# Optimization experiments

Hardware: AMD Instinct MI355X
Metric: run time of the kernel (lower is better)

Reference implementation:

```python
import jax, jax.numpy as jnp
import numpy as np

H, KV, D, HID = 36, 4, 128, 4608   # heads, kv heads, head_dim, hidden
THETA = 100000.0
NEG = -1e30


def _rope_neox(pos, x):
    # pos: [T] int, x: [T, nh, D]; neox style: rotate half
    half = D // 2
    inv_freq = 1.0 / (THETA ** (jnp.arange(half, dtype=jnp.float32) / half))
    ang = pos.astype(jnp.float32)[:, None] * inv_freq          # [T, half]
    cos = jnp.cos(ang)[:, None, :]
    sin = jnp.sin(ang)[:, None, :]
    x1, x2 = x[..., :half], x[..., half:]
    return jnp.concatenate([x1 * cos - x2 * sin, x2 * cos + x1 * sin], axis=-1)


def setup_inputs() -> dict:
    key = jax.random.key(0)
    ks = jax.random.split(key, 6)
    T = 2048
    return {
        "positions": jnp.arange(T, dtype=jnp.int32),
        "hidden_states": jax.random.normal(ks[0], (T, HID), dtype=jnp.float32),
        "wqkv": jax.random.normal(ks[1], (H * D + 2 * KV * D, HID), dtype=jnp.float32) * 0.02,
        "bqkv": jax.random.normal(ks[2], (H * D + 2 * KV * D,), dtype=jnp.float32) * 0.02,
        "wo": jax.random.normal(ks[3], (HID, H * D), dtype=jnp.float32) * 0.02,
        "bo": jax.random.normal(ks[4], (HID,), dtype=jnp.float32) * 0.02,
        "window": 1024,
    }


def reference(positions, hidden_states, wqkv, bqkv, wo, bo, window):
    T = hidden_states.shape[0]
    qkv = hidden_states @ wqkv.T + bqkv                         # [T, 5632]
    q, k, v = jnp.split(qkv, [H * D, H * D + KV * D], axis=-1)
    q = q.reshape(T, H, D)
    k = k.reshape(T, KV, D)
    v = v.reshape(T, KV, D)
    q = _rope_neox(positions, q)
    k = _rope_neox(positions, k)
    # GQA: expand kv heads to query heads
    g = H // KV
    k = jnp.repeat(k, g, axis=1)                                # [T, H, D]
    v = jnp.repeat(v, g, axis=1)
    scale = D ** -0.5
    scores = jnp.einsum('thd,shd->hts', q, k) * scale           # [H, T, T]
    t = jnp.arange(T)
    # causal + sliding window: attend to s in (t - window, t]
    mask = (t[None, :] <= t[:, None]) & (t[None, :] > t[:, None] - window)
    scores = jnp.where(mask[None, :, :], scores, NEG)
    p = jax.nn.softmax(scores, axis=-1)
    attn = jnp.einsum('hts,shd->thd', p, v).reshape(T, H * D)
    return attn @ wo.T + bo
```

## Files before the change

### kernel.cpp

```cpp
#include <hip/hip_runtime.h>
#include <hip/hip_bf16.h>
#include <math.h>


#define T_SEQ   2048
#define HIDDEN  4608
#define NHEAD   36
#define NKVH    4
#define HEADDIM 128
#define GQA_G   9
#define NQKV    5632
#define KOFF    4608
#define VOFF    5120
#define NEG_BIG -1e30f
#define BQ 64
#define BS 32
#define NTILE   64
#define PSTR 40

typedef short bf16x8 __attribute__((ext_vector_type(8)));
typedef float f32x4  __attribute__((ext_vector_type(4)));

__device__ inline bf16x8 pack8(float4 u, float4 v) {
    union { bf16x8 v8; __hip_bfloat162 h[4]; } r;
    r.h[0] = __float22bfloat162_rn(make_float2(u.x, u.y));
    r.h[1] = __float22bfloat162_rn(make_float2(u.z, u.w));
    r.h[2] = __float22bfloat162_rn(make_float2(v.x, v.y));
    r.h[3] = __float22bfloat162_rn(make_float2(v.z, v.w));
    return r.v8;
}

typedef const __attribute__((address_space(1))) int* gas_ptr;
typedef __attribute__((address_space(3))) int*       las_ptr;
__device__ __forceinline__ void gload_lds16(const void* g, void* l) {
    __builtin_amdgcn_global_load_lds((gas_ptr)g, (las_ptr)l, 16, 0, 0);
}

__global__ __launch_bounds__(256)
void cvt_bf16_kernel(const float* __restrict__ in, __hip_bfloat16* __restrict__ out,
                     int n8)
{
    for (int i = blockIdx.x * 256 + threadIdx.x; i < n8; i += gridDim.x * 256) {
        const float4 a = *(const float4*)(in + (size_t)i * 8);
        const float4 b = *(const float4*)(in + (size_t)i * 8 + 4);
        *(bf16x8*)(out + (size_t)i * 8) = pack8(a, b);
    }
}

__global__ __launch_bounds__(256)
void gemm_bf16bt_kernel(const __hip_bfloat16* __restrict__ A,
                        const __hip_bfloat16* __restrict__ B,
                        const float* __restrict__ bias,
                        float* __restrict__ C, int N, int K)
{
    __shared__ short As[128 * 32];
    __shared__ short Bs[128 * 32];

    const int tid  = threadIdx.x;
    const int lane = tid & 63;
    const int wave = tid >> 6;
    const int row0 = blockIdx.y * 128;
    const int col0 = blockIdx.x * 128;
    const int wr   = (wave >> 1) * 64;
    const int wc   = (wave & 1) * 64;
    const int fr   = lane & 15;
    const int fk   = (lane >> 4) * 8;

    const int srow = lane >> 2;
    const int scol = (lane & 3) * 8;

    const __hip_bfloat16* Ag0 = A + (size_t)(row0 + wave * 32 + srow) * K + scol;
    const __hip_bfloat16* Ag1 = Ag0 + (size_t)16 * K;
    const __hip_bfloat16* Bg0 = B + (size_t)(col0 + wave * 32 + srow) * K + scol;
    const __hip_bfloat16* Bg1 = Bg0 + (size_t)16 * K;

    short* Al0 = &As[(wave * 32) * 32];
    short* Al1 = &As[(wave * 32 + 16) * 32];
    short* Bl0 = &Bs[(wave * 32) * 32];
    short* Bl1 = &Bs[(wave * 32 + 16) * 32];

    f32x4 acc[4][4];
    #pragma unroll
    for (int i = 0; i < 4; ++i)
        #pragma unroll
        for (int j = 0; j < 4; ++j)
            #pragma unroll
            for (int r = 0; r < 4; ++r) acc[i][j][r] = 0.0f;

    for (int k0 = 0; k0 < K; k0 += 32) {
        __syncthreads();
        gload_lds16(Ag0 + k0, Al0);
        gload_lds16(Ag1 + k0, Al1);
        gload_lds16(Bg0 + k0, Bl0);
        gload_lds16(Bg1 + k0, Bl1);
        __syncthreads();

        bf16x8 af[4], bfr[4];
        #pragma unroll
        for (int i = 0; i < 4; ++i)
            af[i] = *(const bf16x8*)&As[(wr + i * 16 + fr) * 32 + fk];
        #pragma unroll
        for (int j = 0; j < 4; ++j)
            bfr[j] = *(const bf16x8*)&Bs[(wc + j * 16 + fr) * 32 + fk];

        #pragma unroll
        for (int i = 0; i < 4; ++i)
            #pragma unroll
            for (int j = 0; j < 4; ++j)
                acc[i][j] = __builtin_amdgcn_mfma_f32_16x16x32_bf16(
                    af[i], bfr[j], acc[i][j], 0, 0, 0);
    }

    const int quad = lane >> 4;
    #pragma unroll
    for (int j = 0; j < 4; ++j) {
        const int col = col0 + wc + j * 16 + fr;
        const float bv = bias[col];
        #pragma unroll
        for (int i = 0; i < 4; ++i) {
            const int rowb = row0 + wr + i * 16 + quad * 4;
            #pragma unroll
            for (int r = 0; r < 4; ++r)
                C[(size_t)(rowb + r) * N + col] = acc[i][j][r] + bv;
        }
    }
}

__global__ __launch_bounds__(256)
void prep_kv_kernel(const int* __restrict__ positions,
                    const float* __restrict__ qkv,
                    __hip_bfloat16* __restrict__ Kht,
                    __hip_bfloat16* __restrict__ Klt,
                    __hip_bfloat16* __restrict__ Vtt)
{
    const int tile = blockIdx.x;
    const int kvh  = blockIdx.y;
    const int t    = threadIdx.x;
    const size_t ib = ((size_t)kvh * NTILE + tile) * 4096;

    {
        const int s   = t >> 3;
        const int j8  = (t & 7) * 8;
        const int row = tile * BS + s;
        const float* kp = qkv + (size_t)row * NQKV + KOFF + kvh * HEADDIM;
        float x1[8], x2[8];
        *(float4*)&x1[0] = *(const float4*)(kp + j8);
        *(float4*)&x1[4] = *(const float4*)(kp + j8 + 4);
        *(float4*)&x2[0] = *(const float4*)(kp + 64 + j8);
        *(float4*)&x2[4] = *(const float4*)(kp + 64 + j8 + 4);
        const float pos = (float)positions[row];
        union { bf16x8 v; __hip_bfloat16 x[8]; } H1, L1, H2, L2;
        #pragma unroll
        for (int j = 0; j < 8; ++j) {
            const int d = j8 + j;
            const float inv_freq = __expf(-(float)d * (11.512925465f / 64.0f));
            float sn, cs;
            sincosf(pos * inv_freq, &sn, &cs);
            const float r1 = x1[j] * cs - x2[j] * sn;
            const float r2 = x2[j] * cs + x1[j] * sn;
            const __hip_bfloat16 h1 = __float2bfloat16(r1);
            const __hip_bfloat16 h2 = __float2bfloat16(r2);
            H1.x[j] = h1; L1.x[j] = __float2bfloat16(r1 - __bfloat162float(h1));
            H2.x[j] = h2; L2.x[j] = __float2bfloat16(r2 - __bfloat162float(h2));
        }
        const int gd1 = (t & 7);
        const int gd2 = gd1 + 8;
        *(bf16x8*)&Kht[ib + gd1 * 256 + s * 8] = H1.v;
        *(bf16x8*)&Kht[ib + gd2 * 256 + s * 8] = H2.v;
        *(bf16x8*)&Klt[ib + gd1 * 256 + s * 8] = L1.v;
        *(bf16x8*)&Klt[ib + gd2 * 256 + s * 8] = L2.v;
    }

    {
        const int q  = t >> 6;
        const int d0 = (t & 63) * 2;
        const float* vp = qkv + (size_t)(tile * BS + q * 8) * NQKV + VOFF
                        + kvh * HEADDIM + d0;
        union { bf16x8 v; __hip_bfloat16 x[8]; } V0, V1;
        #pragma unroll
        for (int j = 0; j < 8; ++j) {
            const float2 vv = *(const float2*)(vp + (size_t)j * NQKV);
            const __hip_bfloat162 pb = __float22bfloat162_rn(make_float2(vv.x, vv.y));
            V0.x[j] = pb.x;
            V1.x[j] = pb.y;
        }
        *(bf16x8*)&Vtt[ib + q * 1024 + d0 * 8]       = V0.v;
        *(bf16x8*)&Vtt[ib + q * 1024 + (d0 + 1) * 8] = V1.v;
    }
}

__global__ __launch_bounds__(256)
void attn_kernel(const float* __restrict__ qkv,
                 const int* __restrict__ positions,
                 const __hip_bfloat16* __restrict__ Kht,
                 const __hip_bfloat16* __restrict__ Klt,
                 const __hip_bfloat16* __restrict__ Vtt,
                 __hip_bfloat16* __restrict__ out,
                 const int* __restrict__ windowp)
{
    __shared__ short KhS[2][4096];
    __shared__ short KlS[2][4096];
    __shared__ short VtS[2][4096];
    __shared__ __hip_bfloat16 Ps[4][16 * PSTR];

    const int h    = blockIdx.x;
    const int q0   = blockIdx.y * BQ;
    const int kvh  = h / GQA_G;
    const int tid  = threadIdx.x;
    const int lane = tid & 63;
    const int wave = tid >> 6;
    const int l15  = lane & 15;
    const int quad = lane >> 4;
    const int window = *windowp;
    const float scale = 0.088388347648318447f;

    bf16x8 qh[4], ql[4];
    {
        const int qrow = q0 + wave * 16 + l15;
        const float* qp = qkv + (size_t)qrow * NQKV + h * HEADDIM + quad * 8;
        float qv[32];
        #pragma unroll
        for (int ks = 0; ks < 4; ++ks) {
            *(float4*)&qv[ks * 8]     = *(const float4*)(qp + ks * 32);
            *(float4*)&qv[ks * 8 + 4] = *(const float4*)(qp + ks * 32 + 4);
        }
        const float pos = (float)positions[qrow];
        #pragma unroll
        for (int p = 0; p < 2; ++p)
            #pragma unroll
            for (int j = 0; j < 8; ++j) {
                const int d = p * 32 + quad * 8 + j;
                const float inv_freq = __expf(-(float)d * (11.512925465f / 64.0f));
                float sn, cs;
                sincosf(pos * inv_freq, &sn, &cs);
                const float x1 = qv[p * 8 + j];
                const float x2 = qv[(p + 2) * 8 + j];
                qv[p * 8 + j]       = x1 * cs - x2 * sn;
                qv[(p + 2) * 8 + j] = x2 * cs + x1 * sn;
            }
        #pragma unroll
        for (int ks = 0; ks < 4; ++ks) {
            union { bf16x8 v; __hip_bfloat16 x[8]; } H, L;
            #pragma unroll
            for (int j = 0; j < 8; ++j) {
                const float v = qv[ks * 8 + j] * scale;
                const __hip_bfloat16 hb = __float2bfloat16(v);
                H.x[j] = hb;
                L.x[j] = __float2bfloat16(v - __bfloat162float(hb));
            }
            qh[ks] = H.v; ql[ks] = L.v;
        }
    }

    f32x4 o[8];
    #pragma unroll
    for (int c = 0; c < 8; ++c)
        #pragma unroll
        for (int r = 0; r < 4; ++r) o[c][r] = 0.0f;
    float mrun[4], lrun[4];
    #pragma unroll
    for (int r = 0; r < 4; ++r) { mrun[r] = NEG_BIG; lrun[r] = 0.0f; }

    int s_lo = q0 - window + 1;
    if (s_lo < 0) s_lo = 0;
    s_lo &= ~(BS - 1);
    const int tile0  = s_lo >> 5;
    const int ntiles = ((q0 + BQ) - s_lo) >> 5;

    const short* gKh = (const short*)Kht + ((size_t)kvh * NTILE) * 4096;
    const short* gKl = (const short*)Klt + ((size_t)kvh * NTILE) * 4096;
    const short* gVt = (const short*)Vtt + ((size_t)kvh * NTILE) * 4096;

    __hip_bfloat16* Psw = &Ps[wave][0];

    auto STAGE = [&](int buf, int tile) {
        const size_t toff = (size_t)tile * 4096;
        #pragma unroll
        for (int i = 0; i < 2; ++i) {
            const int o = (wave * 2 + i) * 512;
            gload_lds16(gKh + toff + o + lane * 8, &KhS[buf][o]);
            gload_lds16(gKl + toff + o + lane * 8, &KlS[buf][o]);
            gload_lds16(gVt + toff + o + lane * 8, &VtS[buf][o]);
        }
    };

    STAGE(0, tile0);
    __syncthreads();
    int cur = 0;

    for (int it = 0; it < ntiles; ++it) {
        const int st = s_lo + it * BS;
        if (it + 1 < ntiles) STAGE(cur ^ 1, tile0 + it + 1);

        f32x4 acc0, acc1;
        #pragma unroll
        for (int r = 0; r < 4; ++r) { acc0[r] = 0.0f; acc1[r] = 0.0f; }
        #pragma unroll
        for (int ks = 0; ks < 4; ++ks) {
            const int g = (ks * 4 + quad) * 256;
            const bf16x8 bh0 = *(const bf16x8*)&KhS[cur][g + l15 * 8];
            const bf16x8 bl0 = *(const bf16x8*)&KlS[cur][g + l15 * 8];
            const bf16x8 bh1 = *(const bf16x8*)&KhS[cur][g + (16 + l15) * 8];
            const bf16x8 bl1 = *(const bf16x8*)&KlS[cur][g + (16 + l15) * 8];
            acc0 = __builtin_amdgcn_mfma_f32_16x16x32_bf16(qh[ks], bh0, acc0, 0, 0, 0);
            acc1 = __builtin_amdgcn_mfma_f32_16x16x32_bf16(qh[ks], bh1, acc1, 0, 0, 0);
            acc0 = __builtin_amdgcn_mfma_f32_16x16x32_bf16(ql[ks], bh0, acc0, 0, 0, 0);
            acc1 = __builtin_amdgcn_mfma_f32_16x16x32_bf16(ql[ks], bh1, acc1, 0, 0, 0);
            acc0 = __builtin_amdgcn_mfma_f32_16x16x32_bf16(qh[ks], bl0, acc0, 0, 0, 0);
            acc1 = __builtin_amdgcn_mfma_f32_16x16x32_bf16(qh[ks], bl1, acc1, 0, 0, 0);
        }

        const int qb  = q0 + wave * 16 + quad * 4;
        const int s0g = st + l15;
        const int s1g = st + 16 + l15;
        #pragma unroll
        for (int r = 0; r < 4; ++r) {
            const int q = qb + r;
            const bool v0 = (s0g <= q) && (s0g > q - window);
            const bool v1 = (s1g <= q) && (s1g > q - window);
            float a = v0 ? acc0[r] : NEG_BIG;
            float b = v1 ? acc1[r] : NEG_BIG;
            float mx = fmaxf(a, b);
            mx = fmaxf(mx, __shfl_xor(mx, 1));
            mx = fmaxf(mx, __shfl_xor(mx, 2));
            mx = fmaxf(mx, __shfl_xor(mx, 4));
            mx = fmaxf(mx, __shfl_xor(mx, 8));
            mx = fmaxf(mrun[r], mx);
            const float alpha = __expf(mrun[r] - mx);
            mrun[r] = mx;
            const float e0 = v0 ? __expf(acc0[r] - mx) : 0.0f;
            const float e1 = v1 ? __expf(acc1[r] - mx) : 0.0f;
            const __hip_bfloat162 pp = __float22bfloat162_rn(make_float2(e0, e1));
            Psw[(quad * 4 + r) * PSTR + l15]      = pp.x;
            Psw[(quad * 4 + r) * PSTR + 16 + l15] = pp.y;
            float sum = __bfloat162float(pp.x) + __bfloat162float(pp.y);
            sum += __shfl_xor(sum, 1);
            sum += __shfl_xor(sum, 2);
            sum += __shfl_xor(sum, 4);
            sum += __shfl_xor(sum, 8);
            lrun[r] = lrun[r] * alpha + sum;
            #pragma unroll
            for (int c = 0; c < 8; ++c) o[c][r] *= alpha;
        }

        const bf16x8 pa = *(const bf16x8*)&Psw[l15 * PSTR + quad * 8];
        #pragma unroll
        for (int c = 0; c < 8; ++c) {
            const bf16x8 vb = *(const bf16x8*)&VtS[cur][quad * 1024 + (16 * c + l15) * 8];
            o[c] = __builtin_amdgcn_mfma_f32_16x16x32_bf16(pa, vb, o[c], 0, 0, 0);
        }

        __syncthreads();
        cur ^= 1;
    }

    #pragma unroll
    for (int r = 0; r < 4; ++r) {
        const float inv = 1.0f / lrun[r];
        __hip_bfloat16* op = out
                  + (size_t)(q0 + wave * 16 + quad * 4 + r) * (NHEAD * HEADDIM)
                  + h * HEADDIM + l15;
        #pragma unroll
        for (int c = 0; c < 8; ++c) op[16 * c] = __float2bfloat16(o[c][r] * inv);
    }
}

extern "C" void kernel_launch(void* const* d_in, const int* in_sizes, int n_in,
                              void* d_out, int out_size, void* d_ws, size_t ws_size,
                              hipStream_t stream)
{
    const int*   positions = (const int*)d_in[0];
    const float* hidden    = (const float*)d_in[1];
    const float* wqkv      = (const float*)d_in[2];
    const float* bqkv      = (const float*)d_in[3];
    const float* wo        = (const float*)d_in[4];
    const float* bo        = (const float*)d_in[5];
    const int*   windowp   = (const int*)d_in[6];
    float* outp = (float*)d_out;

    float* qkv = (float*)d_ws;
    __hip_bfloat16* hbf  = (__hip_bfloat16*)(qkv + (size_t)T_SEQ * NQKV);
    __hip_bfloat16* wqbf = hbf  + (size_t)T_SEQ * HIDDEN;
    __hip_bfloat16* wobf = wqbf + (size_t)NQKV * HIDDEN;
    __hip_bfloat16* abf  = wobf + (size_t)HIDDEN * HIDDEN;
    __hip_bfloat16* Kht  = abf  + (size_t)T_SEQ * HIDDEN;
    __hip_bfloat16* Klt  = Kht  + (size_t)NKVH * NTILE * 4096;
    __hip_bfloat16* Vtt  = Klt  + (size_t)NKVH * NTILE * 4096;

    cvt_bf16_kernel<<<1024, 256, 0, stream>>>(hidden, hbf, T_SEQ * HIDDEN / 8);
    cvt_bf16_kernel<<<2048, 256, 0, stream>>>(wqkv, wqbf, NQKV * HIDDEN / 8);
    cvt_bf16_kernel<<<2048, 256, 0, stream>>>(wo, wobf, HIDDEN * HIDDEN / 8);

    gemm_bf16bt_kernel<<<dim3(NQKV / 128, T_SEQ / 128), 256, 0, stream>>>(
        hbf, wqbf, bqkv, qkv, NQKV, HIDDEN);

    prep_kv_kernel<<<dim3(NTILE, NKVH), 256, 0, stream>>>(
        positions, qkv, Kht, Klt, Vtt);

    attn_kernel<<<dim3(NHEAD, T_SEQ / BQ), 256, 0, stream>>>(
        qkv, positions, Kht, Klt, Vtt, abf, windowp);

    gemm_bf16bt_kernel<<<dim3(HIDDEN / 128, T_SEQ / 128), 256, 0, stream>>>(
        abf, wobf, bo, outp, HIDDEN, HIDDEN);
}
```

Baseline: 717.8 us.

## Switch attention to fp16 single-pass MFMA, lazy rescale, and deepen GEMM K-step

Attention drops the bf16 hi/lo split of Q and K, which needed three MFMAs per product, and uses a single fp16 MFMA instead. It also folds log2(e) into the scale to use exp2, and skips the online-softmax rescale unless the row max grows by more than a threshold. The attention grid is reversed so the heaviest query blocks launch first, and the GEMM now loads 64 K-elements per barrier pair using two LDS buffers. The fp16 path trades accuracy for speed, with overflow risk if values exceed the fp16 range, and the lazy rescale lets exponentials reach up to 2^8 before renormalising.

```diff
diff --git a/kernel.cpp b/kernel.cpp
--- a/kernel.cpp
+++ b/kernel.cpp
@@ -18,8 +18,9 @@
 #define NTILE   64
 #define PSTR 40
 
-typedef short bf16x8 __attribute__((ext_vector_type(8)));
-typedef float f32x4  __attribute__((ext_vector_type(4)));
+typedef short    bf16x8 __attribute__((ext_vector_type(8)));
+typedef _Float16 f16x8  __attribute__((ext_vector_type(8)));
+typedef float    f32x4  __attribute__((ext_vector_type(4)));
 
 __device__ inline bf16x8 pack8(float4 u, float4 v) {
     union { bf16x8 v8; __hip_bfloat162 h[4]; } r;
@@ -53,8 +54,8 @@
                         const float* __restrict__ bias,
                         float* __restrict__ C, int N, int K)
 {
-    __shared__ short As[128 * 32];
-    __shared__ short Bs[128 * 32];
+    __shared__ short As[2][128 * 32];
+    __shared__ short Bs[2][128 * 32];
 
     const int tid  = threadIdx.x;
     const int lane = tid & 63;
@@ -69,15 +70,8 @@
     const int srow = lane >> 2;
     const int scol = (lane & 3) * 8;
 
-    const __hip_bfloat16* Ag0 = A + (size_t)(row0 + wave * 32 + srow) * K + scol;
-    const __hip_bfloat16* Ag1 = Ag0 + (size_t)16 * K;
-    const __hip_bfloat16* Bg0 = B + (size_t)(col0 + wave * 32 + srow) * K + scol;
-    const __hip_bfloat16* Bg1 = Bg0 + (size_t)16 * K;
-
-    short* Al0 = &As[(wave * 32) * 32];
-    short* Al1 = &As[(wave * 32 + 16) * 32];
-    short* Bl0 = &Bs[(wave * 32) * 32];
-    short* Bl1 = &Bs[(wave * 32 + 16) * 32];
+    const __hip_bfloat16* Ag = A + (size_t)(row0 + wave * 32 + srow) * K + scol;
+    const __hip_bfloat16* Bg = B + (size_t)(col0 + wave * 32 + srow) * K + scol;
 
     f32x4 acc[4][4];
     #pragma unroll
@@ -87,28 +81,36 @@
             #pragma unroll
             for (int r = 0; r < 4; ++r) acc[i][j][r] = 0.0f;
 
-    for (int k0 = 0; k0 < K; k0 += 32) {
+    for (int k0 = 0; k0 < K; k0 += 64) {
         __syncthreads();
-        gload_lds16(Ag0 + k0, Al0);
-        gload_lds16(Ag1 + k0, Al1);
-        gload_lds16(Bg0 + k0, Bl0);
-        gload_lds16(Bg1 + k0, Bl1);
+        #pragma unroll
+        for (int kk = 0; kk < 2; ++kk)
+            #pragma unroll
+            for (int i = 0; i < 2; ++i) {
+                gload_lds16(Ag + k0 + kk * 32 + (size_t)(i * 16) * K,
+                            &As[kk][(wave * 32 + i * 16) * 32]);
+                gload_lds16(Bg + k0 + kk * 32 + (size_t)(i * 16) * K,
+                            &Bs[kk][(wave * 32 + i * 16) * 32]);
+            }
         __syncthreads();
 
-        bf16x8 af[4], bfr[4];
-        #pragma unroll
-        for (int i = 0; i < 4; ++i)
-            af[i] = *(const bf16x8*)&As[(wr + i * 16 + fr) * 32 + fk];
-        #pragma unroll
-        for (int j = 0; j < 4; ++j)
-            bfr[j] = *(const bf16x8*)&Bs[(wc + j * 16 + fr) * 32 + fk];
-
-        #pragma unroll
-        for (int i = 0; i < 4; ++i)
+        #pragma unroll
+        for (int kk = 0; kk < 2; ++kk) {
+            bf16x8 af[4], bfr[4];
+            #pragma unroll
+            for (int i = 0; i < 4; ++i)
+                af[i] = *(const bf16x8*)&As[kk][(wr + i * 16 + fr) * 32 + fk];
             #pragma unroll
             for (int j = 0; j < 4; ++j)
-                acc[i][j] = __builtin_amdgcn_mfma_f32_16x16x32_bf16(
-                    af[i], bfr[j], acc[i][j], 0, 0, 0);
+                bfr[j] = *(const bf16x8*)&Bs[kk][(wc + j * 16 + fr) * 32 + fk];
+
+            #pragma unroll
+            for (int i = 0; i < 4; ++i)
+                #pragma unroll
+                for (int j = 0; j < 4; ++j)
+                    acc[i][j] = __builtin_amdgcn_mfma_f32_16x16x32_bf16(
+                        af[i], bfr[j], acc[i][j], 0, 0, 0);
+        }
     }
 
     const int quad = lane >> 4;
@@ -129,9 +131,8 @@
 __global__ __launch_bounds__(256)
 void prep_kv_kernel(const int* __restrict__ positions,
                     const float* __restrict__ qkv,
-                    __hip_bfloat16* __restrict__ Kht,
-                    __hip_bfloat16* __restrict__ Klt,
-                    __hip_bfloat16* __restrict__ Vtt)
+                    _Float16* __restrict__ Kt,
+                    _Float16* __restrict__ Vt)
 {
     const int tile = blockIdx.x;
     const int kvh  = blockIdx.y;
@@ -149,26 +150,20 @@
         *(float4*)&x2[0] = *(const float4*)(kp + 64 + j8);
         *(float4*)&x2[4] = *(const float4*)(kp + 64 + j8 + 4);
         const float pos = (float)positions[row];
-        union { bf16x8 v; __hip_bfloat16 x[8]; } H1, L1, H2, L2;
+        f16x8 H1, H2;
         #pragma unroll
         for (int j = 0; j < 8; ++j) {
             const int d = j8 + j;
             const float inv_freq = __expf(-(float)d * (11.512925465f / 64.0f));
             float sn, cs;
             sincosf(pos * inv_freq, &sn, &cs);
-            const float r1 = x1[j] * cs - x2[j] * sn;
-            const float r2 = x2[j] * cs + x1[j] * sn;
-            const __hip_bfloat16 h1 = __float2bfloat16(r1);
-            const __hip_bfloat16 h2 = __float2bfloat16(r2);
-            H1.x[j] = h1; L1.x[j] = __float2bfloat16(r1 - __bfloat162float(h1));
-            H2.x[j] = h2; L2.x[j] = __float2bfloat16(r2 - __bfloat162float(h2));
+            H1[j] = (_Float16)(x1[j] * cs - x2[j] * sn);
+            H2[j] = (_Float16)(x2[j] * cs + x1[j] * sn);
         }
         const int gd1 = (t & 7);
         const int gd2 = gd1 + 8;
-        *(bf16x8*)&Kht[ib + gd1 * 256 + s * 8] = H1.v;
-        *(bf16x8*)&Kht[ib + gd2 * 256 + s * 8] = H2.v;
-        *(bf16x8*)&Klt[ib + gd1 * 256 + s * 8] = L1.v;
-        *(bf16x8*)&Klt[ib + gd2 * 256 + s * 8] = L2.v;
+        *(f16x8*)&Kt[ib + gd1 * 256 + s * 8] = H1;
+        *(f16x8*)&Kt[ib + gd2 * 256 + s * 8] = H2;
     }
 
     {
@@ -176,35 +171,32 @@
         const int d0 = (t & 63) * 2;
         const float* vp = qkv + (size_t)(tile * BS + q * 8) * NQKV + VOFF
                         + kvh * HEADDIM + d0;
-        union { bf16x8 v; __hip_bfloat16 x[8]; } V0, V1;
+        f16x8 V0, V1;
         #pragma unroll
         for (int j = 0; j < 8; ++j) {
             const float2 vv = *(const float2*)(vp + (size_t)j * NQKV);
-            const __hip_bfloat162 pb = __float22bfloat162_rn(make_float2(vv.x, vv.y));
-            V0.x[j] = pb.x;
-            V1.x[j] = pb.y;
-        }
-        *(bf16x8*)&Vtt[ib + q * 1024 + d0 * 8]       = V0.v;
-        *(bf16x8*)&Vtt[ib + q * 1024 + (d0 + 1) * 8] = V1.v;
+            V0[j] = (_Float16)vv.x;
+            V1[j] = (_Float16)vv.y;
+        }
+        *(f16x8*)&Vt[ib + q * 1024 + d0 * 8]       = V0;
+        *(f16x8*)&Vt[ib + q * 1024 + (d0 + 1) * 8] = V1;
     }
 }
 
 __global__ __launch_bounds__(256)
 void attn_kernel(const float* __restrict__ qkv,
                  const int* __restrict__ positions,
-                 const __hip_bfloat16* __restrict__ Kht,
-                 const __hip_bfloat16* __restrict__ Klt,
-                 const __hip_bfloat16* __restrict__ Vtt,
+                 const _Float16* __restrict__ Kt,
+                 const _Float16* __restrict__ Vt,
                  __hip_bfloat16* __restrict__ out,
                  const int* __restrict__ windowp)
 {
-    __shared__ short KhS[2][4096];
-    __shared__ short KlS[2][4096];
-    __shared__ short VtS[2][4096];
-    __shared__ __hip_bfloat16 Ps[4][16 * PSTR];
+    __shared__ _Float16 KS[2][4096];
+    __shared__ _Float16 VS[2][4096];
+    __shared__ _Float16 Ps[4][16 * PSTR];
 
     const int h    = blockIdx.x;
-    const int q0   = blockIdx.y * BQ;
+    const int q0   = (T_SEQ / BQ - 1 - blockIdx.y) * BQ;
     const int kvh  = h / GQA_G;
     const int tid  = threadIdx.x;
     const int lane = tid & 63;
@@ -212,9 +204,9 @@
     const int l15  = lane & 15;
     const int quad = lane >> 4;
     const int window = *windowp;
-    const float scale = 0.088388347648318447f;
-
-    bf16x8 qh[4], ql[4];
+    const float scale = 0.088388347648318447f * 1.4426950408889634f;
+
+    f16x8 qf[4];
     {
         const int qrow = q0 + wave * 16 + l15;
         const float* qp = qkv + (size_t)qrow * NQKV + h * HEADDIM + quad * 8;
@@ -239,17 +231,10 @@
                 qv[(p + 2) * 8 + j] = x2 * cs + x1 * sn;
             }
         #pragma unroll
-        for (int ks = 0; ks < 4; ++ks) {
-            union { bf16x8 v; __hip_bfloat16 x[8]; } H, L;
-            #pragma unroll
-            for (int j = 0; j < 8; ++j) {
-                const float v = qv[ks * 8 + j] * scale;
-                const __hip_bfloat16 hb = __float2bfloat16(v);
-                H.x[j] = hb;
-                L.x[j] = __float2bfloat16(v - __bfloat162float(hb));
-            }
-            qh[ks] = H.v; ql[ks] = L.v;
-        }
+        for (int ks = 0; ks < 4; ++ks)
+            #pragma unroll
+            for (int j = 0; j < 8; ++j)
+                qf[ks][j] = (_Float16)(qv[ks * 8 + j] * scale);
     }
 
     f32x4 o[8];
@@ -267,20 +252,18 @@
     const int tile0  = s_lo >> 5;
     const int ntiles = ((q0 + BQ) - s_lo) >> 5;
 
-    const short* gKh = (const short*)Kht + ((size_t)kvh * NTILE) * 4096;
-    const short* gKl = (const short*)Klt + ((size_t)kvh * NTILE) * 4096;
-    const short* gVt = (const short*)Vtt + ((size_t)kvh * NTILE) * 4096;
-
-    __hip_bfloat16* Psw = &Ps[wave][0];
+    const _Float16* gK = Kt + ((size_t)kvh * NTILE) * 4096;
+    const _Float16* gV = Vt + ((size_t)kvh * NTILE) * 4096;
+
+    _Float16* Psw = &Ps[wave][0];
 
     auto STAGE = [&](int buf, int tile) {
         const size_t toff = (size_t)tile * 4096;
         #pragma unroll
         for (int i = 0; i < 2; ++i) {
             const int o = (wave * 2 + i) * 512;
-            gload_lds16(gKh + toff + o + lane * 8, &KhS[buf][o]);
-            gload_lds16(gKl + toff + o + lane * 8, &KlS[buf][o]);
-            gload_lds16(gVt + toff + o + lane * 8, &VtS[buf][o]);
+            gload_lds16(gK + toff + o + lane * 8, &KS[buf][o]);
+            gload_lds16(gV + toff + o + lane * 8, &VS[buf][o]);
         }
     };
 
@@ -298,16 +281,10 @@
         #pragma unroll
         for (int ks = 0; ks < 4; ++ks) {
             const int g = (ks * 4 + quad) * 256;
-            const bf16x8 bh0 = *(const bf16x8*)&KhS[cur][g + l15 * 8];
-            const bf16x8 bl0 = *(const bf16x8*)&KlS[cur][g + l15 * 8];
-            const bf16x8 bh1 = *(const bf16x8*)&KhS[cur][g + (16 + l15) * 8];
-            const bf16x8 bl1 = *(const bf16x8*)&KlS[cur][g + (16 + l15) * 8];
-            acc0 = __builtin_amdgcn_mfma_f32_16x16x32_bf16(qh[ks], bh0, acc0, 0, 0, 0);
-            acc1 = __builtin_amdgcn_mfma_f32_16x16x32_bf16(qh[ks], bh1, acc1, 0, 0, 0);
-            acc0 = __builtin_amdgcn_mfma_f32_16x16x32_bf16(ql[ks], bh0, acc0, 0, 0, 0);
-            acc1 = __builtin_amdgcn_mfma_f32_16x16x32_bf16(ql[ks], bh1, acc1, 0, 0, 0);
-            acc0 = __builtin_amdgcn_mfma_f32_16x16x32_bf16(qh[ks], bl0, acc0, 0, 0, 0);
-            acc1 = __builtin_amdgcn_mfma_f32_16x16x32_bf16(qh[ks], bl1, acc1, 0, 0, 0);
+            const f16x8 b0 = *(const f16x8*)&KS[cur][g + l15 * 8];
+            const f16x8 b1 = *(const f16x8*)&KS[cur][g + (16 + l15) * 8];
+            acc0 = __builtin_amdgcn_mfma_f32_16x16x32_f16(qf[ks], b0, acc0, 0, 0, 0);
+            acc1 = __builtin_amdgcn_mfma_f32_16x16x32_f16(qf[ks], b1, acc1, 0, 0, 0);
         }
 
         const int qb  = q0 + wave * 16 + quad * 4;
@@ -325,29 +302,33 @@
             mx = fmaxf(mx, __shfl_xor(mx, 2));
             mx = fmaxf(mx, __shfl_xor(mx, 4));
             mx = fmaxf(mx, __shfl_xor(mx, 8));
-            mx = fmaxf(mrun[r], mx);
-            const float alpha = __expf(mrun[r] - mx);
-            mrun[r] = mx;
-            const float e0 = v0 ? __expf(acc0[r] - mx) : 0.0f;
-            const float e1 = v1 ? __expf(acc1[r] - mx) : 0.0f;
-            const __hip_bfloat162 pp = __float22bfloat162_rn(make_float2(e0, e1));
-            Psw[(quad * 4 + r) * PSTR + l15]      = pp.x;
-            Psw[(quad * 4 + r) * PSTR + 16 + l15] = pp.y;
-            float sum = __bfloat162float(pp.x) + __bfloat162float(pp.y);
+            if (__any(mx > mrun[r] + 8.0f)) {
+                const float mnew  = fmaxf(mrun[r], mx);
+                const float alpha = __builtin_amdgcn_exp2f(mrun[r] - mnew);
+                mrun[r] = mnew;
+                lrun[r] *= alpha;
+                #pragma unroll
+                for (int c = 0; c < 8; ++c) o[c][r] *= alpha;
+            }
+            const float e0 = v0 ? __builtin_amdgcn_exp2f(acc0[r] - mrun[r]) : 0.0f;
+            const float e1 = v1 ? __builtin_amdgcn_exp2f(acc1[r] - mrun[r]) : 0.0f;
+            const _Float16 p0 = (_Float16)e0;
+            const _Float16 p1 = (_Float16)e1;
+            Psw[(quad * 4 + r) * PSTR + l15]      = p0;
+            Psw[(quad * 4 + r) * PSTR + 16 + l15] = p1;
+            float sum = (float)p0 + (float)p1;
             sum += __shfl_xor(sum, 1);
             sum += __shfl_xor(sum, 2);
             sum += __shfl_xor(sum, 4);
             sum += __shfl_xor(sum, 8);
-            lrun[r] = lrun[r] * alpha + sum;
-            #pragma unroll
-            for (int c = 0; c < 8; ++c) o[c][r] *= alpha;
-        }
-
-        const bf16x8 pa = *(const bf16x8*)&Psw[l15 * PSTR + quad * 8];
+            lrun[r] += sum;
+        }
+
+        const f16x8 pa = *(const f16x8*)&Psw[l15 * PSTR + quad * 8];
         #pragma unroll
         for (int c = 0; c < 8; ++c) {
-            const bf16x8 vb = *(const bf16x8*)&VtS[cur][quad * 1024 + (16 * c + l15) * 8];
-            o[c] = __builtin_amdgcn_mfma_f32_16x16x32_bf16(pa, vb, o[c], 0, 0, 0);
+            const f16x8 vb = *(const f16x8*)&VS[cur][quad * 1024 + (16 * c + l15) * 8];
+            o[c] = __builtin_amdgcn_mfma_f32_16x16x32_f16(pa, vb, o[c], 0, 0, 0);
         }
 
         __syncthreads();
@@ -383,9 +364,8 @@
     __hip_bfloat16* wqbf = hbf  + (size_t)T_SEQ * HIDDEN;
     __hip_bfloat16* wobf = wqbf + (size_t)NQKV * HIDDEN;
     __hip_bfloat16* abf  = wobf + (size_t)HIDDEN * HIDDEN;
-    __hip_bfloat16* Kht  = abf  + (size_t)T_SEQ * HIDDEN;
-    __hip_bfloat16* Klt  = Kht  + (size_t)NKVH * NTILE * 4096;
-    __hip_bfloat16* Vtt  = Klt  + (size_t)NKVH * NTILE * 4096;
+    _Float16*       Kt   = (_Float16*)(abf + (size_t)T_SEQ * HIDDEN);
+    _Float16*       Vt   = Kt + (size_t)NKVH * NTILE * 4096;
 
     cvt_bf16_kernel<<<1024, 256, 0, stream>>>(hidden, hbf, T_SEQ * HIDDEN / 8);
     cvt_bf16_kernel<<<2048, 256, 0, stream>>>(wqkv, wqbf, NQKV * HIDDEN / 8);
@@ -395,10 +375,10 @@
         hbf, wqbf, bqkv, qkv, NQKV, HIDDEN);
 
     prep_kv_kernel<<<dim3(NTILE, NKVH), 256, 0, stream>>>(
-        positions, qkv, Kht, Klt, Vtt);
+        positions, qkv, Kt, Vt);
 
     attn_kernel<<<dim3(NHEAD, T_SEQ / BQ), 256, 0, stream>>>(
-        qkv, positions, Kht, Klt, Vtt, abf, windowp);
+        qkv, positions, Kt, Vt, abf, windowp);
 
     gemm_bf16bt_kernel<<<dim3(HIDDEN / 128, T_SEQ / 128), 256, 0, stream>>>(
         abf, wobf, bo, outp, HIDDEN, HIDDEN);
```

After: 790.1 us. 1.1x slower.
